# Kernel optimization log

Hardware: AMD Instinct MI355X
Metric: run time of the kernel (lower is better)

Reference implementation:

```python
import jax, jax.numpy as jnp
import numpy as np

D_MODEL = 1024
NUM_HEADS = 16
HEAD_DIM = D_MODEL // NUM_HEADS
B, S = 2, 2048


def setup_inputs() -> dict:
    key = jax.random.key(0)
    ks = jax.random.split(key, 6)
    scale = 0.02
    return {
        "x": jax.random.normal(ks[0], (B, S, D_MODEL), dtype=jnp.float32),
        "mask": jax.random.normal(ks[1], (S, S), dtype=jnp.float32),
        "Wqkv": jax.random.normal(ks[2], (D_MODEL, 3 * D_MODEL), dtype=jnp.float32) * scale,
        "bqkv": jax.random.normal(ks[3], (3 * D_MODEL,), dtype=jnp.float32) * scale,
        "Wout": jax.random.normal(ks[4], (D_MODEL, D_MODEL), dtype=jnp.float32) * scale,
        "bout": jax.random.normal(ks[5], (D_MODEL,), dtype=jnp.float32) * scale,
    }


def reference(x, mask, Wqkv, bqkv, Wout, bout):
    b, s, d = x.shape
    h, hd = NUM_HEADS, HEAD_DIM
    qkv = x @ Wqkv + bqkv                              # [b, s, 3d]
    qkv = qkv.reshape(b, s, h, 3 * hd).transpose(0, 2, 1, 3)  # [b, h, s, 3hd]
    q, k, v = jnp.split(qkv, 3, axis=-1)               # each [b, h, s, hd]
    scaled = jnp.einsum("bhqd,bhkd->bhqk", q, k) / jnp.sqrt(jnp.float32(hd))
    scaled = scaled + mask                             # mask [s, s] broadcasts
    attn = jax.nn.softmax(scaled, axis=-1)
    values = jnp.einsum("bhqk,bhkd->bhqd", attn, v)    # [b, h, s, hd]
    values = values.transpose(0, 2, 1, 3).reshape(b, s, d)
    return values @ Wout + bout
```

## Files before the change

kernel.cpp:

```cpp
#include <hip/hip_runtime.h>
#include <hip/hip_bf16.h>

#define D_MODEL 1024
#define NH 16
#define HD 64
#define BATCH 2
#define SEQ 2048
#define M_TOTAL (BATCH*SEQ)

typedef _Float16 f16;
typedef _Float16 half8 __attribute__((ext_vector_type(8)));
typedef _Float16 half4v __attribute__((ext_vector_type(4)));
typedef float floatx4 __attribute__((ext_vector_type(4)));

__device__ inline void gload_lds16(const void* g, void* l) {
    __builtin_amdgcn_global_load_lds(
        (const __attribute__((address_space(1))) unsigned int*)g,
        (__attribute__((address_space(3))) unsigned int*)l, 16, 0, 0);
}

__global__ void cvt_f32_f16(const float* __restrict__ src, f16* __restrict__ dst, int n4) {
    int i = blockIdx.x * blockDim.x + threadIdx.x;
    if (i < n4) {
        float4 v = ((const float4*)src)[i];
        half4v o = { (f16)v.x, (f16)v.y, (f16)v.z, (f16)v.w };
        *(half4v*)(dst + (long)i * 4) = o;
    }
}

__global__ void exp_cvt(const float* __restrict__ src, f16* __restrict__ dst, int n4) {
    int i = blockIdx.x * blockDim.x + threadIdx.x;
    if (i < n4) {
        float4 v = ((const float4*)src)[i];
        half4v o = { (f16)__expf(v.x), (f16)__expf(v.y), (f16)__expf(v.z), (f16)__expf(v.w) };
        *(half4v*)(dst + (long)i * 4) = o;
    }
}

__global__ void transpose_cvt(const float* __restrict__ src, f16* __restrict__ dst, int R, int C) {
    __shared__ float tile[32][33];
    int tx = threadIdx.x;
    int ty = threadIdx.y;
    int c0 = blockIdx.x * 32;
    int r0 = blockIdx.y * 32;
    for (int yy = 0; yy < 32; yy += 8)
        tile[ty + yy][tx] = src[(long)(r0 + ty + yy) * C + c0 + tx];
    __syncthreads();
    for (int yy = 0; yy < 32; yy += 8)
        dst[(long)(c0 + ty + yy) * R + r0 + tx] = (f16)tile[tx][ty + yy];
}

template<int MODE, int TN>
__global__ __launch_bounds__(256) void gemm_mfma(
    const f16* __restrict__ A, const f16* __restrict__ BT,
    const float* __restrict__ bias,
    f16* __restrict__ Qh, f16* __restrict__ Kh, f16* __restrict__ Vtg,
    float* __restrict__ out, int Kdim)
{
    constexpr int NF = TN / 32;
    __shared__ f16 Ah[128 * 64];
    __shared__ f16 Bh[TN * 64];
    int tid  = threadIdx.x;
    int wid  = tid >> 6;
    int lane = tid & 63;
    int quad = lane >> 4;
    int l16  = lane & 15;
    int m0 = blockIdx.y * 128;
    int n0 = blockIdx.x * TN;
    int mrow = (wid >> 1) * 64;
    int ncol = (wid & 1) * (TN / 2);
    int grow = lane >> 3;
    int gchunk = (lane & 7) ^ (grow & 7);
    int sw0 = ((quad)     ^ (l16 & 7)) * 8;
    int sw1 = ((quad + 4) ^ (l16 & 7)) * 8;

    floatx4 acc[4][NF];
    #pragma unroll
    for (int mb = 0; mb < 4; mb++)
        #pragma unroll
        for (int nb = 0; nb < NF; nb++) acc[mb][nb] = (floatx4){0.f, 0.f, 0.f, 0.f};

    const f16* Abase = A + (long)m0 * Kdim;
    const f16* Bbase = BT + (long)n0 * Kdim;

    for (int k0 = 0; k0 < Kdim; k0 += 64) {
        #pragma unroll
        for (int j = 0; j < 4; j++) {
            int r = j * 32 + wid * 8 + grow;
            gload_lds16(Abase + (long)r * Kdim + k0 + gchunk * 8, &Ah[(j * 32 + wid * 8) * 64]);
        }
        #pragma unroll
        for (int j = 0; j < TN / 32; j++) {
            int r = j * 32 + wid * 8 + grow;
            gload_lds16(Bbase + (long)r * Kdim + k0 + gchunk * 8, &Bh[(j * 32 + wid * 8) * 64]);
        }
        __syncthreads();
        #pragma unroll
        for (int h = 0; h < 2; h++) {
            int sw = h ? sw1 : sw0;
            half8 af[4];
            #pragma unroll
            for (int mb = 0; mb < 4; mb++)
                af[mb] = *(const half8*)&Ah[(mrow + mb * 16 + l16) * 64 + sw];
            #pragma unroll
            for (int nb = 0; nb < NF; nb++) {
                half8 bf = *(const half8*)&Bh[(ncol + nb * 16 + l16) * 64 + sw];
                #pragma unroll
                for (int mb = 0; mb < 4; mb++)
                    acc[mb][nb] = __builtin_amdgcn_mfma_f32_16x16x32_f16(af[mb], bf, acc[mb][nb], 0, 0, 0);
            }
        }
        __syncthreads();
    }

    #pragma unroll
    for (int nb = 0; nb < NF; nb++) {
        int n = n0 + ncol + nb * 16 + l16;
        float bv = bias[n];
        int head = 0, t = 0, d = 0;
        if (MODE == 0) { head = n / 192; int rem = n % 192; t = rem / 64; d = rem % 64; }
        #pragma unroll
        for (int mb = 0; mb < 4; mb++) {
            int mbase = m0 + mrow + mb * 16 + quad * 4;
            if (MODE == 0) {
                int b = mbase >> 11;
                int s = mbase & 2047;
                long bh = b * NH + head;
                if (t == 2) {
                    half4v pack;
                    #pragma unroll
                    for (int r = 0; r < 4; r++) pack[r] = (f16)(acc[mb][nb][r] + bv);
                    *(half4v*)&Vtg[(bh * HD + d) * SEQ + s] = pack;
                } else if (t == 0) {
                    #pragma unroll
                    for (int r = 0; r < 4; r++)
                        Qh[(bh * SEQ + s + r) * HD + d] = (f16)((acc[mb][nb][r] + bv) * 0.125f);
                } else {
                    #pragma unroll
                    for (int r = 0; r < 4; r++)
                        Kh[(bh * SEQ + s + r) * HD + d] = (f16)(acc[mb][nb][r] + bv);
                }
            } else {
                #pragma unroll
                for (int r = 0; r < 4; r++)
                    out[(long)(mbase + r) * D_MODEL + n] = acc[mb][nb][r] + bv;
            }
        }
    }
}

__global__ __launch_bounds__(256) void attn(
    const f16* __restrict__ Qh, const f16* __restrict__ Kh, const f16* __restrict__ Vtg,
    const f16* __restrict__ E, f16* __restrict__ valh)
{
    __shared__ f16 Kl[64 * 64];
    __shared__ f16 Vt[64 * 64];
    __shared__ f16 Pl[4][32 * 68];
    int tid  = threadIdx.x;
    int wid  = tid >> 6;
    int lane = tid & 63;
    int quad = lane >> 4;
    int l16  = lane & 15;
    int bh = blockIdx.y;
    int b  = bh >> 4;
    int h  = bh & 15;
    int q0 = blockIdx.x * 128 + wid * 32;

    int grow = lane >> 3;
    int gchunk = (lane & 7) ^ (grow & 7);
    int sw0 = ((quad)     ^ (l16 & 7)) * 8;
    int sw1 = ((quad + 4) ^ (l16 & 7)) * 8;

    const f16* Qbase = Qh + ((long)bh * SEQ + q0) * HD;
    half8 qf[2][2];
    #pragma unroll
    for (int m = 0; m < 2; m++)
        #pragma unroll
        for (int c = 0; c < 2; c++)
            qf[m][c] = *(const half8*)&Qbase[(long)(m * 16 + l16) * HD + c * 32 + quad * 8];

    floatx4 Of[2][4];
    float sums[2][4];
    #pragma unroll
    for (int m = 0; m < 2; m++) {
        #pragma unroll
        for (int nb = 0; nb < 4; nb++) Of[m][nb] = (floatx4){0.f, 0.f, 0.f, 0.f};
        #pragma unroll
        for (int r = 0; r < 4; r++) sums[m][r] = 0.f;
    }

    const f16* Kb = Kh + (long)bh * SEQ * HD;
    const f16* Vb = Vtg + (long)bh * HD * SEQ;

    for (int k0 = 0; k0 < SEQ; k0 += 64) {
        __syncthreads();
        #pragma unroll
        for (int j = 0; j < 2; j++) {
            int r = j * 32 + wid * 8 + grow;
            gload_lds16(Kb + (long)(k0 + r) * HD + gchunk * 8, &Kl[(j * 32 + wid * 8) * 64]);
            gload_lds16(Vb + (long)r * SEQ + k0 + gchunk * 8, &Vt[(j * 32 + wid * 8) * 64]);
        }
        __syncthreads();

        f16 ef[2][4][4];
        #pragma unroll
        for (int m = 0; m < 2; m++)
            #pragma unroll
            for (int r = 0; r < 4; r++) {
                const f16* Erow = E + (long)(q0 + m * 16 + quad * 4 + r) * SEQ + k0 + l16;
                #pragma unroll
                for (int kb = 0; kb < 4; kb++) ef[m][r][kb] = Erow[kb * 16];
            }

        floatx4 sc[2][4];
        #pragma unroll
        for (int kb = 0; kb < 4; kb++) {
            half8 kf0 = *(const half8*)&Kl[(kb * 16 + l16) * 64 + sw0];
            half8 kf1 = *(const half8*)&Kl[(kb * 16 + l16) * 64 + sw1];
            #pragma unroll
            for (int m = 0; m < 2; m++) {
                floatx4 s = (floatx4){0.f, 0.f, 0.f, 0.f};
                s = __builtin_amdgcn_mfma_f32_16x16x32_f16(qf[m][0], kf0, s, 0, 0, 0);
                s = __builtin_amdgcn_mfma_f32_16x16x32_f16(qf[m][1], kf1, s, 0, 0, 0);
                sc[m][kb] = s;
            }
        }

        #pragma unroll
        for (int m = 0; m < 2; m++)
            #pragma unroll
            for (int kb = 0; kb < 4; kb++)
                #pragma unroll
                for (int r = 0; r < 4; r++) {
                    float p = (float)ef[m][r][kb] * __expf(sc[m][kb][r]);
                    sums[m][r] += p;
                    Pl[wid][(m * 16 + quad * 4 + r) * 68 + kb * 16 + l16] = (f16)p;
                }

        half8 pf[2][2];
        #pragma unroll
        for (int m = 0; m < 2; m++)
            #pragma unroll
            for (int c = 0; c < 2; c++)
                pf[m][c] = *(const half8*)&Pl[wid][(m * 16 + l16) * 68 + c * 32 + quad * 8];

        #pragma unroll
        for (int nb = 0; nb < 4; nb++) {
            half8 vf0 = *(const half8*)&Vt[(nb * 16 + l16) * 64 + sw0];
            half8 vf1 = *(const half8*)&Vt[(nb * 16 + l16) * 64 + sw1];
            #pragma unroll
            for (int m = 0; m < 2; m++) {
                Of[m][nb] = __builtin_amdgcn_mfma_f32_16x16x32_f16(pf[m][0], vf0, Of[m][nb], 0, 0, 0);
                Of[m][nb] = __builtin_amdgcn_mfma_f32_16x16x32_f16(pf[m][1], vf1, Of[m][nb], 0, 0, 0);
            }
        }
    }

    #pragma unroll
    for (int m = 0; m < 2; m++)
        #pragma unroll
        for (int r = 0; r < 4; r++) {
            float s = sums[m][r];
            s += __shfl_xor(s, 1);
            s += __shfl_xor(s, 2);
            s += __shfl_xor(s, 4);
            s += __shfl_xor(s, 8);
            sums[m][r] = 1.f / s;
        }

    #pragma unroll
    for (int m = 0; m < 2; m++)
        #pragma unroll
        for (int nb = 0; nb < 4; nb++)
            #pragma unroll
            for (int r = 0; r < 4; r++) {
                int q = q0 + m * 16 + quad * 4 + r;
                int d = nb * 16 + l16;
                valh[((long)(b * SEQ + q)) * D_MODEL + h * HD + d] = (f16)(Of[m][nb][r] * sums[m][r]);
            }
}

extern "C" void kernel_launch(void* const* d_in, const int* in_sizes, int n_in,
                              void* d_out, int out_size, void* d_ws, size_t ws_size,
                              hipStream_t stream) {
    const float* x    = (const float*)d_in[0];
    const float* mask = (const float*)d_in[1];
    const float* Wqkv = (const float*)d_in[2];
    const float* bqkv = (const float*)d_in[3];
    const float* Wout = (const float*)d_in[4];
    const float* bout = (const float*)d_in[5];
    float* out = (float*)d_out;

    char* ws = (char*)d_ws;
    f16* xh    = (f16*)(ws + 0);
    f16* E     = (f16*)(ws + 0);
    f16* WqkvT = (f16*)(ws + 8388608);
    f16* WoutT = (f16*)(ws + 14680064);
    f16* Qh    = (f16*)(ws + 16777216);
    f16* Kh    = (f16*)(ws + 25165824);
    f16* Vtg   = (f16*)(ws + 33554432);
    f16* valh  = (f16*)(ws + 41943040);

    cvt_f32_f16<<<4096, 256, 0, stream>>>(x, xh, M_TOTAL * D_MODEL / 4);
    transpose_cvt<<<dim3(96, 32), dim3(32, 8), 0, stream>>>(Wqkv, WqkvT, 1024, 3072);
    transpose_cvt<<<dim3(32, 32), dim3(32, 8), 0, stream>>>(Wout, WoutT, 1024, 1024);
    gemm_mfma<0, 128><<<dim3(24, 32), 256, 0, stream>>>(xh, WqkvT, bqkv, Qh, Kh, Vtg, nullptr, 1024);
    exp_cvt<<<4096, 256, 0, stream>>>(mask, E, SEQ * SEQ / 4);
    attn<<<dim3(16, 32), 256, 0, stream>>>(Qh, Kh, Vtg, E, valh);
    gemm_mfma<1, 64><<<dim3(16, 32), 256, 0, stream>>>(valh, WoutT, bout, nullptr, nullptr, nullptr, out, 1024);
}
```

Baseline: 229.7 us.

## Fuse mask into attention MFMA accumulator and compute row sums via MFMA

Drops the separate exp_cvt pass over the mask. The attention kernel now reads the fp32 mask directly and seeds the QK^T MFMA accumulator with it, using a transposed (K,Q) operand order so the mask tile loads as float4. Row sums are computed by an extra MFMA against a vector of ones instead of scalar accumulation plus shuffles. Blocks shrink to 128 threads with twice as many blocks, and the P tile stride changes to 72. The trade-off is more fp32 mask traffic per block (read by all 32 bh blocks) and extra MFMAs, in exchange for removing a kernel and the fp16 E buffer.

```diff
diff --git a/kernel.cpp b/kernel.cpp
--- a/kernel.cpp
+++ b/kernel.cpp
@@ -24,15 +24,6 @@
     if (i < n4) {
         float4 v = ((const float4*)src)[i];
         half4v o = { (f16)v.x, (f16)v.y, (f16)v.z, (f16)v.w };
-        *(half4v*)(dst + (long)i * 4) = o;
-    }
-}
-
-__global__ void exp_cvt(const float* __restrict__ src, f16* __restrict__ dst, int n4) {
-    int i = blockIdx.x * blockDim.x + threadIdx.x;
-    if (i < n4) {
-        float4 v = ((const float4*)src)[i];
-        half4v o = { (f16)__expf(v.x), (f16)__expf(v.y), (f16)__expf(v.z), (f16)__expf(v.w) };
         *(half4v*)(dst + (long)i * 4) = o;
     }
 }
@@ -149,13 +140,13 @@
     }
 }
 
-__global__ __launch_bounds__(256) void attn(
+__global__ __launch_bounds__(128) void attn(
     const f16* __restrict__ Qh, const f16* __restrict__ Kh, const f16* __restrict__ Vtg,
-    const f16* __restrict__ E, f16* __restrict__ valh)
+    const float* __restrict__ mask, f16* __restrict__ valh)
 {
     __shared__ f16 Kl[64 * 64];
     __shared__ f16 Vt[64 * 64];
-    __shared__ f16 Pl[4][32 * 68];
+    __shared__ f16 Pl[2][32 * 72];
     int tid  = threadIdx.x;
     int wid  = tid >> 6;
     int lane = tid & 63;
@@ -164,10 +155,10 @@
     int bh = blockIdx.y;
     int b  = bh >> 4;
     int h  = bh & 15;
-    int q0 = blockIdx.x * 128 + wid * 32;
-
-    int grow = lane >> 3;
-    int gchunk = (lane & 7) ^ (grow & 7);
+    int q0 = blockIdx.x * 64 + wid * 32;
+
+    int grow8 = lane >> 3;
+    int gpos  = lane & 7;
     int sw0 = ((quad)     ^ (l16 & 7)) * 8;
     int sw1 = ((quad + 4) ^ (l16 & 7)) * 8;
 
@@ -179,14 +170,17 @@
         for (int c = 0; c < 2; c++)
             qf[m][c] = *(const half8*)&Qbase[(long)(m * 16 + l16) * HD + c * 32 + quad * 8];
 
+    half8 vones;
+    #pragma unroll
+    for (int j = 0; j < 8; j++) vones[j] = (f16)1.0f;
+
     floatx4 Of[2][4];
-    float sums[2][4];
+    floatx4 Ofs[2];
     #pragma unroll
     for (int m = 0; m < 2; m++) {
+        Ofs[m] = (floatx4){0.f, 0.f, 0.f, 0.f};
         #pragma unroll
         for (int nb = 0; nb < 4; nb++) Of[m][nb] = (floatx4){0.f, 0.f, 0.f, 0.f};
-        #pragma unroll
-        for (int r = 0; r < 4; r++) sums[m][r] = 0.f;
     }
 
     const f16* Kb = Kh + (long)bh * SEQ * HD;
@@ -195,54 +189,43 @@
     for (int k0 = 0; k0 < SEQ; k0 += 64) {
         __syncthreads();
         #pragma unroll
-        for (int j = 0; j < 2; j++) {
-            int r = j * 32 + wid * 8 + grow;
-            gload_lds16(Kb + (long)(k0 + r) * HD + gchunk * 8, &Kl[(j * 32 + wid * 8) * 64]);
-            gload_lds16(Vb + (long)r * SEQ + k0 + gchunk * 8, &Vt[(j * 32 + wid * 8) * 64]);
-        }
-        __syncthreads();
-
-        f16 ef[2][4][4];
+        for (int j = 0; j < 4; j++) {
+            int rb = j * 16 + wid * 8;
+            int row = rb + grow8;
+            int gk = gpos ^ (row & 7);
+            gload_lds16(Kb + (long)(k0 + row) * HD + gk * 8, &Kl[rb * 64]);
+            gload_lds16(Vb + (long)row * SEQ + k0 + gk * 8, &Vt[rb * 64]);
+        }
+        float4 mk[2][4];
         #pragma unroll
         for (int m = 0; m < 2; m++)
             #pragma unroll
-            for (int r = 0; r < 4; r++) {
-                const f16* Erow = E + (long)(q0 + m * 16 + quad * 4 + r) * SEQ + k0 + l16;
-                #pragma unroll
-                for (int kb = 0; kb < 4; kb++) ef[m][r][kb] = Erow[kb * 16];
-            }
-
-        floatx4 sc[2][4];
+            for (int kb = 0; kb < 4; kb++)
+                mk[m][kb] = *(const float4*)&mask[(long)(q0 + m * 16 + l16) * SEQ + k0 + kb * 16 + quad * 4];
+        __syncthreads();
+
         #pragma unroll
         for (int kb = 0; kb < 4; kb++) {
             half8 kf0 = *(const half8*)&Kl[(kb * 16 + l16) * 64 + sw0];
-            half8 kf1 = *(const half8*)&Kl[(kb * 16 + l16) * 64 + sw1];
+            half8 kf1 = *(const half8*)&Kl[(kb * 16 + l16) * 64 + 32 + sw1 - 32];
             #pragma unroll
             for (int m = 0; m < 2; m++) {
-                floatx4 s = (floatx4){0.f, 0.f, 0.f, 0.f};
-                s = __builtin_amdgcn_mfma_f32_16x16x32_f16(qf[m][0], kf0, s, 0, 0, 0);
-                s = __builtin_amdgcn_mfma_f32_16x16x32_f16(qf[m][1], kf1, s, 0, 0, 0);
-                sc[m][kb] = s;
-            }
-        }
-
+                floatx4 s = (floatx4){mk[m][kb].x, mk[m][kb].y, mk[m][kb].z, mk[m][kb].w};
+                s = __builtin_amdgcn_mfma_f32_16x16x32_f16(kf0, qf[m][0], s, 0, 0, 0);
+                s = __builtin_amdgcn_mfma_f32_16x16x32_f16(kf1, qf[m][1], s, 0, 0, 0);
+                half4v ph;
+                #pragma unroll
+                for (int r = 0; r < 4; r++) ph[r] = (f16)__expf(s[r]);
+                *(half4v*)&Pl[wid][(m * 16 + l16) * 72 + kb * 16 + quad * 4] = ph;
+            }
+        }
+
+        half8 pf[2][2];
         #pragma unroll
         for (int m = 0; m < 2; m++)
             #pragma unroll
-            for (int kb = 0; kb < 4; kb++)
-                #pragma unroll
-                for (int r = 0; r < 4; r++) {
-                    float p = (float)ef[m][r][kb] * __expf(sc[m][kb][r]);
-                    sums[m][r] += p;
-                    Pl[wid][(m * 16 + quad * 4 + r) * 68 + kb * 16 + l16] = (f16)p;
-                }
-
-        half8 pf[2][2];
-        #pragma unroll
-        for (int m = 0; m < 2; m++)
-            #pragma unroll
             for (int c = 0; c < 2; c++)
-                pf[m][c] = *(const half8*)&Pl[wid][(m * 16 + l16) * 68 + c * 32 + quad * 8];
+                pf[m][c] = *(const half8*)&Pl[wid][(m * 16 + l16) * 72 + c * 32 + quad * 8];
 
         #pragma unroll
         for (int nb = 0; nb < 4; nb++) {
@@ -254,30 +237,27 @@
                 Of[m][nb] = __builtin_amdgcn_mfma_f32_16x16x32_f16(pf[m][1], vf1, Of[m][nb], 0, 0, 0);
             }
         }
-    }
-
-    #pragma unroll
-    for (int m = 0; m < 2; m++)
-        #pragma unroll
-        for (int r = 0; r < 4; r++) {
-            float s = sums[m][r];
-            s += __shfl_xor(s, 1);
-            s += __shfl_xor(s, 2);
-            s += __shfl_xor(s, 4);
-            s += __shfl_xor(s, 8);
-            sums[m][r] = 1.f / s;
-        }
-
-    #pragma unroll
-    for (int m = 0; m < 2; m++)
+        #pragma unroll
+        for (int m = 0; m < 2; m++) {
+            Ofs[m] = __builtin_amdgcn_mfma_f32_16x16x32_f16(pf[m][0], vones, Ofs[m], 0, 0, 0);
+            Ofs[m] = __builtin_amdgcn_mfma_f32_16x16x32_f16(pf[m][1], vones, Ofs[m], 0, 0, 0);
+        }
+    }
+
+    #pragma unroll
+    for (int m = 0; m < 2; m++) {
+        floatx4 rs;
+        #pragma unroll
+        for (int r = 0; r < 4; r++) rs[r] = 1.f / Ofs[m][r];
         #pragma unroll
         for (int nb = 0; nb < 4; nb++)
             #pragma unroll
             for (int r = 0; r < 4; r++) {
                 int q = q0 + m * 16 + quad * 4 + r;
                 int d = nb * 16 + l16;
-                valh[((long)(b * SEQ + q)) * D_MODEL + h * HD + d] = (f16)(Of[m][nb][r] * sums[m][r]);
-            }
+                valh[((long)(b * SEQ + q)) * D_MODEL + h * HD + d] = (f16)(Of[m][nb][r] * rs[r]);
+            }
+    }
 }
 
 extern "C" void kernel_launch(void* const* d_in, const int* in_sizes, int n_in,
@@ -293,7 +273,6 @@
 
     char* ws = (char*)d_ws;
     f16* xh    = (f16*)(ws + 0);
-    f16* E     = (f16*)(ws + 0);
     f16* WqkvT = (f16*)(ws + 8388608);
     f16* WoutT = (f16*)(ws + 14680064);
     f16* Qh    = (f16*)(ws + 16777216);
@@ -305,7 +284,6 @@
     transpose_cvt<<<dim3(96, 32), dim3(32, 8), 0, stream>>>(Wqkv, WqkvT, 1024, 3072);
     transpose_cvt<<<dim3(32, 32), dim3(32, 8), 0, stream>>>(Wout, WoutT, 1024, 1024);
     gemm_mfma<0, 128><<<dim3(24, 32), 256, 0, stream>>>(xh, WqkvT, bqkv, Qh, Kh, Vtg, nullptr, 1024);
-    exp_cvt<<<4096, 256, 0, stream>>>(mask, E, SEQ * SEQ / 4);
-    attn<<<dim3(16, 32), 256, 0, stream>>>(Qh, Kh, Vtg, E, valh);
+    attn<<<dim3(32, 32), 128, 0, stream>>>(Qh, Kh, Vtg, mask, valh);
     gemm_mfma<1, 64><<<dim3(16, 32), 256, 0, stream>>>(valh, WoutT, bout, nullptr, nullptr, nullptr, out, 1024);
 }
```

Measured after the change: 258.7 us. +12.6%, slower.
